# Kernel optimization log

Measured on AMD Instinct MI355X. Metric: run time of the kernel, lower is better.

The kernel has to match this reference:

```python
import jax, jax.numpy as jnp
import numpy as np

KERNEL_MUL = 2.0
KERNEL_NUM = 5


def setup_inputs() -> dict:
    key = jax.random.key(0)
    k1, k2 = jax.random.split(key)
    N, D = 8192, 256
    subggroup = jax.random.randint(k1, (N, 1), 0, 2, dtype=jnp.int64)
    outputs = jax.random.normal(k2, (N, D), dtype=jnp.float32)
    return {"subggroup": subggroup, "outputs": outputs}


def reference(subggroup, outputs):
    # Binary labels: rows with label 0 form `source` (Min), label 1 form `target` (Maj).
    # concat(source, target) is a permutation of `outputs`, so we compute the
    # full NxN multi-RBF kernel once and take masked means -- identical math.
    sub = subggroup[:, 0]
    m0 = (sub == 0).astype(outputs.dtype)  # source mask
    m1 = (sub == 1).astype(outputs.dtype)  # target mask
    n = outputs.shape[0]

    # Pairwise squared L2 distances via matmul (fused cdist), [N, N]
    sq = jnp.sum(outputs * outputs, axis=-1)
    L2 = jnp.maximum(sq[:, None] + sq[None, :] - 2.0 * (outputs @ outputs.T), 0.0)

    # bandwidth computed from detached distances (torch uses L2_distance.data)
    bandwidth = jax.lax.stop_gradient(jnp.sum(L2)) / (n * n - n)
    bandwidth = bandwidth / (KERNEL_MUL ** (KERNEL_NUM // 2))

    K = jnp.zeros_like(L2)
    for i in range(KERNEL_NUM):
        K = K + jnp.exp(-L2 / (bandwidth * (KERNEL_MUL ** i)))

    n0 = jnp.sum(m0)
    n1 = jnp.sum(m1)
    XX = jnp.einsum('i,ij,j->', m0, K, m0) / (n0 * n0)
    YY = jnp.einsum('i,ij,j->', m1, K, m1) / (n1 * n1)
    XY = jnp.einsum('i,ij,j->', m0, K, m1) / (n0 * n1)
    YX = jnp.einsum('i,ij,j->', m1, K, m0) / (n1 * n0)
    return XX + YY - XY - YX
```

## Files before the change

kernel.cpp:

```cpp
#include <hip/hip_runtime.h>

#define N_ROWS 8192
#define DIMS   256
#define NTILE  64
#define NFULL  1024
#define NCHUNK 1056
#define K1B    256
#define K3B    512

typedef _Float16 f16x4 __attribute__((ext_vector_type(4)));
typedef _Float16 f16x8 __attribute__((ext_vector_type(8)));
typedef float   f32x16 __attribute__((ext_vector_type(16)));

#define WS_PLANE  0
#define WS_SQ     (4 * 1024 * 1024)
#define WS_RED    (WS_SQ + 32768)
#define WS_SSQA   (WS_RED + 1024)
#define WS_N0A    (WS_SSQA + 4)
#define WS_SC     (WS_N0A + 4)
#define WS_PART   (WS_RED + 2048)

struct Scalars {
    unsigned int ctr;
    unsigned int t3;
};

#define BL(dst, p, o) asm volatile("global_load_dwordx4 %0, %1, off offset:" o \
                                   : "=v"(dst) : "v"(p))

__global__ __launch_bounds__(256) void k1_rows(const float* __restrict__ x,
                                               const long long* __restrict__ sub,
                                               float* __restrict__ sq,
                                               float* __restrict__ colsumA,
                                               float* __restrict__ ssqA,
                                               unsigned int* __restrict__ n0A,
                                               unsigned short* __restrict__ plane) {
    __shared__ _Float16 stg[16 * 512];
    __shared__ float cls[4][256];
    __shared__ float smq[4];
    const int t = threadIdx.x;
    const int l = t & 63;
    const int w = t >> 6;
    const int base = blockIdx.x * 32;

    float4 colacc = make_float4(0.f, 0.f, 0.f, 0.f);
    float  my_sumsq = 0.f;

    const int ks  = l >> 2;
    const int shi = ((l >> 1) & 1) * 32;
    const int j4  = (l & 1) * 4;

    #pragma unroll
    for (int r = 0; r < 8; ++r) {
        const int rr  = w * 8 + r;
        const int row = base + rr;
        const float4 v = ((const float4*)(x + (size_t)row * DIMS))[l];
        colacc.x += v.x; colacc.y += v.y; colacc.z += v.z; colacc.w += v.w;

        f16x4 h = { (_Float16)v.x, (_Float16)v.y, (_Float16)v.z, (_Float16)v.w };
        *(f16x4*)&stg[ks * 512 + (rr + shi) * 8 + j4] = h;

        float s = v.x * v.x + v.y * v.y + v.z * v.z + v.w * v.w;
        #pragma unroll
        for (int off = 32; off; off >>= 1) s += __shfl_down(s, off, 64);
        if (l == 0) { sq[row] = s; my_sumsq += s; }
    }
    if (l == 0) smq[w] = my_sumsq;
    *(float4*)&cls[w][l * 4] = colacc;
    __syncthreads();

    {
        const uint4* src = (const uint4*)stg;
        uint4* dst = (uint4*)(plane + (size_t)blockIdx.x * 8192);
        #pragma unroll
        for (int i = 0; i < 4; ++i) dst[i * 256 + t] = src[i * 256 + t];
    }

    atomicAdd(&colsumA[t], cls[0][t] + cls[1][t] + cls[2][t] + cls[3][t]);
    if (t == 0) atomicAdd(ssqA, smq[0] + smq[1] + smq[2] + smq[3]);
    if (w == 1) {
        unsigned long long m1 = __ballot(l < 32 && (int)sub[base + l] == 0);
        if (l == 0) atomicAdd(n0A, (unsigned int)__popcll(m1));
    }
}

__global__ __launch_bounds__(256, 2) void k3_mmd(const unsigned short* __restrict__ plane,
                                                 const long long* __restrict__ sub,
                                                 const float* __restrict__ sq,
                                                 const float* __restrict__ colsumA,
                                                 const float* __restrict__ ssqA,
                                                 const unsigned int* __restrict__ n0A,
                                                 Scalars* sc,
                                                 double* __restrict__ partial,
                                                 float* __restrict__ out) {
    __shared__ char ldsA[65536];
    __shared__ float2 sqwI[128];
    __shared__ double dd[4];
    __shared__ unsigned int qb;

    const int t  = threadIdx.x;
    const int l  = t & 63;
    const int w  = t >> 6;
    const int lh = l >> 5;
    const int ln = l & 31;

    float c2, w0, w1;
    {
        const float4 c4 = ((const float4*)colsumA)[l];
        float cs2 = c4.x * c4.x + c4.y * c4.y + c4.z * c4.z + c4.w * c4.w;
        #pragma unroll
        for (int off = 32; off; off >>= 1) cs2 += __shfl_xor(cs2, off, 64);
        const float ssq = *ssqA;
        const float n0f = (float)*n0A;
        const double n = (double)N_ROWS;
        const double sumL2 = 2.0 * n * (double)ssq - 2.0 * (double)cs2;
        const double bw = sumL2 / (n * n - n) / 4.0;
        c2 = (float)(-1.4426950408889634 / (16.0 * bw));
        const double n0 = (double)n0f, n1 = n - n0;
        w0 = (float)( 1.0 / n0);
        w1 = (float)(-1.0 / n1);
    }

    double dsum = 0.0;
    f16x8 b[16];

    for (;;) {
        __syncthreads();
        if (t == 0) qb = atomicAdd(&sc->ctr, 1u);
        __syncthreads();
        const unsigned q0 = qb;
        if (q0 >= NCHUNK) break;
        int bi, bj, nt;
        if (q0 < NFULL) {
            int q = (int)q0; bi = 0;
            while (q >= ((NTILE - bi) >> 1)) { q -= (NTILE - bi) >> 1; ++bi; }
            bj = bi + q * 2;
            nt = 2;
        } else {
            bi = 2 * (int)(q0 - NFULL) + 1;
            bj = NTILE - 1;
            nt = 1;
        }

        #pragma unroll
        for (int i = 0; i < 16; ++i) {
            const unsigned short* g = plane + (((size_t)(bi * 4 + w) * 16 + i) << 9) + (l << 3);
            char* lp = ldsA + ((w * 16 + i) << 10);
            __builtin_amdgcn_global_load_lds(
                (const __attribute__((address_space(1))) unsigned int*)(const void*)g,
                (__attribute__((address_space(3))) unsigned int*)(void*)lp, 16, 0, 0);
        }
        if (t < 128) {
            const int I = bi * 128 + t;
            sqwI[t] = make_float2(sq[I], ((int)sub[I] == 0) ? w0 : w1);
        }
        {
            const unsigned short* p0 = plane + (((size_t)(bj * 4 + w) * 16) << 9) + (l << 3);
            const unsigned short* p1 = p0 + 2048;
            const unsigned short* p2 = p0 + 4096;
            const unsigned short* p3 = p0 + 6144;
            BL(b[0], p0,"0"); BL(b[1], p0,"1024"); BL(b[2], p0,"2048"); BL(b[3], p0,"3072");
            BL(b[4], p1,"0"); BL(b[5], p1,"1024"); BL(b[6], p1,"2048"); BL(b[7], p1,"3072");
            BL(b[8], p2,"0"); BL(b[9], p2,"1024"); BL(b[10],p2,"2048"); BL(b[11],p2,"3072");
            BL(b[12],p3,"0"); BL(b[13],p3,"1024"); BL(b[14],p3,"2048"); BL(b[15],p3,"3072");
        }
        const int J0 = bj * 128 + w * 32 + ln;
        float sJ  = sq[J0];
        float wJv = ((int)sub[J0] == 0) ? w0 : w1;
        __syncthreads();

        for (int tt = 0; tt < nt; ++tt, ++bj) {
            const bool dg = (bj == bi);
            asm volatile("s_waitcnt vmcnt(0)" ::: "memory");
            __builtin_amdgcn_sched_barrier(0);

            f32x16 acc[4] = {};
            #pragma unroll
            for (int ks = 0; ks < 16; ++ks) {
                #pragma unroll
                for (int m = 0; m < 4; ++m) {
                    const f16x8 a = *(const f16x8*)(ldsA + ((m * 16 + ks) << 10) + (l << 4));
                    acc[m] = __builtin_amdgcn_mfma_f32_32x32x16_f16(a, b[ks], acc[m], 0, 0, 0);
                }
            }

            float sJn = 0.f, wJn = 0.f;
            if (tt + 1 < nt) {
                const unsigned short* p0 = plane + (((size_t)((bj + 1) * 4 + w) * 16) << 9) + (l << 3);
                const unsigned short* p1 = p0 + 2048;
                const unsigned short* p2 = p0 + 4096;
                const unsigned short* p3 = p0 + 6144;
                BL(b[0], p0,"0"); BL(b[1], p0,"1024"); BL(b[2], p0,"2048"); BL(b[3], p0,"3072");
                BL(b[4], p1,"0"); BL(b[5], p1,"1024"); BL(b[6], p1,"2048"); BL(b[7], p1,"3072");
                BL(b[8], p2,"0"); BL(b[9], p2,"1024"); BL(b[10],p2,"2048"); BL(b[11],p2,"3072");
                BL(b[12],p3,"0"); BL(b[13],p3,"1024"); BL(b[14],p3,"2048"); BL(b[15],p3,"3072");
                const int Jn = (bj + 1) * 128 + w * 32 + ln;
                sJn = sq[Jn];
                wJn = ((int)sub[Jn] == 0) ? w0 : w1;
            }

            float part = 0.f;
            #pragma unroll
            for (int m = 0; m < 4; ++m) {
                #pragma unroll
                for (int r = 0; r < 16; ++r) {
                    const int Il = m * 32 + (r & 3) + ((r >> 2) << 3) + (lh << 2);
                    const float2 pi = sqwI[Il];
                    float l2 = fmaxf(pi.x + sJ - 2.f * acc[m][r], 0.f);
                    const float e  = __builtin_amdgcn_exp2f(l2 * c2);
                    const float e2 = e * e, e4 = e2 * e2, e8 = e4 * e4;
                    const float K  = ((e + e2) + (e4 + e8)) + e8 * e8;
                    float w2 = pi.y * wJv;
                    if (dg) {
                        const int Jl = w * 32 + ln;
                        w2 *= (Il < Jl) ? 2.f : ((Il == Jl) ? 1.f : 0.f);
                    }
                    part = fmaf(K, w2, part);
                }
            }
            dsum += (double)part * (dg ? 1.0 : 2.0);
            sJ = sJn; wJv = wJn;
        }
    }

    #pragma unroll
    for (int off = 32; off; off >>= 1) dsum += __shfl_down(dsum, off, 64);
    __syncthreads();
    if (l == 0) dd[w] = dsum;
    __syncthreads();
    if (t == 0) {
        partial[blockIdx.x] = dd[0] + dd[1] + dd[2] + dd[3];
        __threadfence();
        qb = (atomicAdd(&sc->t3, 1u) == K3B - 1) ? 1u : 0u;
    }
    __syncthreads();
    if (qb) {
        __threadfence();
        double v = partial[t] + partial[t + 256];
        #pragma unroll
        for (int off = 32; off; off >>= 1) v += __shfl_down(v, off, 64);
        if (l == 0) dd[w] = v;
        __syncthreads();
        if (t == 0) out[0] = (float)(dd[0] + dd[1] + dd[2] + dd[3]);
    }
}

extern "C" void kernel_launch(void* const* d_in, const int* in_sizes, int n_in,
                              void* d_out, int out_size, void* d_ws, size_t ws_size,
                              hipStream_t stream) {
    const long long* sub = (const long long*)d_in[0];
    const float*     x   = (const float*)d_in[1];
    float* out = (float*)d_out;

    char* ws = (char*)d_ws;
    unsigned short* plane   = (unsigned short*)(ws + WS_PLANE);
    float*          sq      = (float*)(ws + WS_SQ);
    float*          colsumA = (float*)(ws + WS_RED);
    float*          ssqA    = (float*)(ws + WS_SSQA);
    unsigned int*   n0A     = (unsigned int*)(ws + WS_N0A);
    Scalars*        sc      = (Scalars*)(ws + WS_SC);
    double*         partial = (double*)(ws + WS_PART);

    hipMemsetAsync(ws + WS_RED, 0, 1040, stream);
    k1_rows<<<K1B, 256, 0, stream>>>(x, sub, sq, colsumA, ssqA, n0A, plane);
    k3_mmd<<<K3B, 256, 0, stream>>>(plane, sub, sq, colsumA, ssqA, n0A, sc, partial, out);
}
```

Measured before the change: 120.0 us.

## Halve row tile to 64 rows, double chunks and blocks, prefetch work counter

```diff
diff --git a/kernel.cpp b/kernel.cpp
--- a/kernel.cpp
+++ b/kernel.cpp
@@ -2,11 +2,12 @@
 
 #define N_ROWS 8192
 #define DIMS   256
-#define NTILE  64
-#define NFULL  1024
-#define NCHUNK 1056
+#define NRT    128
+#define NCT    64
+#define NFULL  2048
+#define NCHUNK 2112
 #define K1B    256
-#define K3B    512
+#define K3B    1024
 
 typedef _Float16 f16x4 __attribute__((ext_vector_type(4)));
 typedef _Float16 f16x8 __attribute__((ext_vector_type(8)));
@@ -93,8 +94,8 @@
                                                  Scalars* sc,
                                                  double* __restrict__ partial,
                                                  float* __restrict__ out) {
-    __shared__ char ldsA[65536];
-    __shared__ float2 sqwI[128];
+    __shared__ char ldsA[32768];
+    __shared__ float2 sqwI[64];
     __shared__ double dd[4];
     __shared__ unsigned int qb;
 
@@ -124,38 +125,39 @@
     double dsum = 0.0;
     f16x8 b[16];
 
+    if (t == 0) qb = atomicAdd(&sc->ctr, 1u);
     for (;;) {
-        __syncthreads();
-        if (t == 0) qb = atomicAdd(&sc->ctr, 1u);
         __syncthreads();
         const unsigned q0 = qb;
         if (q0 >= NCHUNK) break;
-        int bi, bj, nt;
+        int ri, cj, nt;
         if (q0 < NFULL) {
-            int q = (int)q0; bi = 0;
-            while (q >= ((NTILE - bi) >> 1)) { q -= (NTILE - bi) >> 1; ++bi; }
-            bj = bi + q * 2;
+            int q = (int)q0; ri = 0;
+            for (;;) { const int fc = (NCT - (ri >> 1)) >> 1; if (q < fc) break; q -= fc; ++ri; }
+            cj = (ri >> 1) + 2 * q;
             nt = 2;
         } else {
-            bi = 2 * (int)(q0 - NFULL) + 1;
-            bj = NTILE - 1;
+            const int s = (int)(q0 - NFULL);
+            const int bb = 2 * (s >> 1) + 1;
+            ri = 2 * bb + (s & 1);
+            cj = NCT - 1;
             nt = 1;
         }
 
         #pragma unroll
-        for (int i = 0; i < 16; ++i) {
-            const unsigned short* g = plane + (((size_t)(bi * 4 + w) * 16 + i) << 9) + (l << 3);
-            char* lp = ldsA + ((w * 16 + i) << 10);
+        for (int i = 0; i < 8; ++i) {
+            const unsigned short* g = plane + (((size_t)(ri * 32 + w * 8 + i)) << 9) + (l << 3);
+            char* lp = ldsA + ((w * 8 + i) << 10);
             __builtin_amdgcn_global_load_lds(
                 (const __attribute__((address_space(1))) unsigned int*)(const void*)g,
                 (__attribute__((address_space(3))) unsigned int*)(void*)lp, 16, 0, 0);
         }
-        if (t < 128) {
-            const int I = bi * 128 + t;
+        if (t < 64) {
+            const int I = ri * 64 + t;
             sqwI[t] = make_float2(sq[I], ((int)sub[I] == 0) ? w0 : w1);
         }
         {
-            const unsigned short* p0 = plane + (((size_t)(bj * 4 + w) * 16) << 9) + (l << 3);
+            const unsigned short* p0 = plane + (((size_t)(cj * 4 + w) * 16) << 9) + (l << 3);
             const unsigned short* p1 = p0 + 2048;
             const unsigned short* p2 = p0 + 4096;
             const unsigned short* p3 = p0 + 6144;
@@ -164,29 +166,32 @@
             BL(b[8], p2,"0"); BL(b[9], p2,"1024"); BL(b[10],p2,"2048"); BL(b[11],p2,"3072");
             BL(b[12],p3,"0"); BL(b[13],p3,"1024"); BL(b[14],p3,"2048"); BL(b[15],p3,"3072");
         }
-        const int J0 = bj * 128 + w * 32 + ln;
+        const int J0 = cj * 128 + w * 32 + ln;
         float sJ  = sq[J0];
         float wJv = ((int)sub[J0] == 0) ? w0 : w1;
         __syncthreads();
 
-        for (int tt = 0; tt < nt; ++tt, ++bj) {
-            const bool dg = (bj == bi);
+        for (int tt = 0; tt < nt; ++tt) {
+            const int cjt = cj + tt;
+            const bool dg = (cjt == (ri >> 1));
             asm volatile("s_waitcnt vmcnt(0)" ::: "memory");
             __builtin_amdgcn_sched_barrier(0);
 
-            f32x16 acc[4] = {};
+            f32x16 acc[2] = {};
             #pragma unroll
             for (int ks = 0; ks < 16; ++ks) {
                 #pragma unroll
-                for (int m = 0; m < 4; ++m) {
+                for (int m = 0; m < 2; ++m) {
                     const f16x8 a = *(const f16x8*)(ldsA + ((m * 16 + ks) << 10) + (l << 4));
                     acc[m] = __builtin_amdgcn_mfma_f32_32x32x16_f16(a, b[ks], acc[m], 0, 0, 0);
                 }
             }
 
+            if (tt == nt - 1 && t == 0) qb = atomicAdd(&sc->ctr, 1u);
+
             float sJn = 0.f, wJn = 0.f;
             if (tt + 1 < nt) {
-                const unsigned short* p0 = plane + (((size_t)((bj + 1) * 4 + w) * 16) << 9) + (l << 3);
+                const unsigned short* p0 = plane + (((size_t)((cjt + 1) * 4 + w) * 16) << 9) + (l << 3);
                 const unsigned short* p1 = p0 + 2048;
                 const unsigned short* p2 = p0 + 4096;
                 const unsigned short* p3 = p0 + 6144;
@@ -194,14 +199,14 @@
                 BL(b[4], p1,"0"); BL(b[5], p1,"1024"); BL(b[6], p1,"2048"); BL(b[7], p1,"3072");
                 BL(b[8], p2,"0"); BL(b[9], p2,"1024"); BL(b[10],p2,"2048"); BL(b[11],p2,"3072");
                 BL(b[12],p3,"0"); BL(b[13],p3,"1024"); BL(b[14],p3,"2048"); BL(b[15],p3,"3072");
-                const int Jn = (bj + 1) * 128 + w * 32 + ln;
+                const int Jn = (cjt + 1) * 128 + w * 32 + ln;
                 sJn = sq[Jn];
                 wJn = ((int)sub[Jn] == 0) ? w0 : w1;
             }
 
             float part = 0.f;
             #pragma unroll
-            for (int m = 0; m < 4; ++m) {
+            for (int m = 0; m < 2; ++m) {
                 #pragma unroll
                 for (int r = 0; r < 16; ++r) {
                     const int Il = m * 32 + (r & 3) + ((r >> 2) << 3) + (lh << 2);
@@ -212,8 +217,9 @@
                     const float K  = ((e + e2) + (e4 + e8)) + e8 * e8;
                     float w2 = pi.y * wJv;
                     if (dg) {
-                        const int Jl = w * 32 + ln;
-                        w2 *= (Il < Jl) ? 2.f : ((Il == Jl) ? 1.f : 0.f);
+                        const int Ig = ri * 64 + Il;
+                        const int Jg = cjt * 128 + w * 32 + ln;
+                        w2 *= (Ig < Jg) ? 2.f : ((Ig == Jg) ? 1.f : 0.f);
                     }
                     part = fmaf(K, w2, part);
                 }
@@ -236,7 +242,7 @@
     __syncthreads();
     if (qb) {
         __threadfence();
-        double v = partial[t] + partial[t + 256];
+        double v = partial[t] + partial[t + 256] + partial[t + 512] + partial[t + 768];
         #pragma unroll
         for (int off = 32; off; off >>= 1) v += __shfl_down(v, off, 64);
         if (l == 0) dd[w] = v;
```

New measurement: 138.7 us. +15.6%, slower.
